# Kernel tuning notes

Hardware: AMD Instinct MI355X
Metric: run time of the kernel (lower is better)

The kernel has to match this reference:

```python
import jax, jax.numpy as jnp
import numpy as np

NEG_SLOPE = 0.2
EPS = 1e-16

N_NODES = 100000
N_EDGES = 1600000
IN_CH = 128
HEADS = 4
OUT_CH = 32


def setup_inputs() -> dict:
    key = jax.random.key(0)
    k1, k2, k3, k4, k5 = jax.random.split(key, 5)
    x = jax.random.normal(k1, (N_NODES, IN_CH), dtype=jnp.float32)
    edge_index = jax.random.randint(k2, (2, N_EDGES), 0, N_NODES, dtype=jnp.int64)
    glorot = (6.0 / (IN_CH + HEADS * OUT_CH)) ** 0.5
    W_l = jax.random.uniform(k3, (IN_CH, HEADS * OUT_CH), jnp.float32, -glorot, glorot)
    W_r = jax.random.uniform(k4, (IN_CH, HEADS * OUT_CH), jnp.float32, -glorot, glorot)
    ga = (6.0 / (OUT_CH + 1)) ** 0.5
    att = jax.random.uniform(k5, (HEADS, OUT_CH), jnp.float32, -ga, ga)
    bias = jnp.zeros((HEADS * OUT_CH,), dtype=jnp.float32)
    return {"x": x, "edge_index": edge_index, "W_l": W_l, "W_r": W_r, "att": att, "bias": bias}


def reference(x, edge_index, W_l, W_r, att, bias):
    # GATv2Conv forward (PyG semantics, concat=True, add_self_loops=False)
    N = x.shape[0]
    H, C = att.shape
    src, dst = edge_index[0], edge_index[1]

    x_l = (x @ W_l).reshape(N, H, C)  # source transform
    x_r = (x @ W_r).reshape(N, H, C)  # target transform

    # per-edge attention logits: e_ij = att . leaky_relu(x_l[j] + x_r[i])
    h = x_l[src] + x_r[dst]                      # [E, H, C]
    e = jnp.einsum('ehc,hc->eh', jax.nn.leaky_relu(h, NEG_SLOPE), att)  # [E, H]

    # segment softmax over edges grouped by destination node
    m = jax.ops.segment_max(e, dst, num_segments=N)      # [N, H]
    e_exp = jnp.exp(e - m[dst])                          # [E, H]
    denom = jax.ops.segment_sum(e_exp, dst, num_segments=N)  # [N, H]
    alpha = e_exp / (denom[dst] + EPS)                   # [E, H]

    # attention-weighted message aggregation
    msg = x_l[src] * alpha[:, :, None]                   # [E, H, C]
    out = jax.ops.segment_sum(msg, dst, num_segments=N)  # [N, H, C]
    return out.reshape(N, H * C) + bias
```

## Files before the change

### kernel.cpp

```cpp
#include <hip/hip_runtime.h>
#include <hip/hip_bf16.h>
#include <cstdint>
#include <cstddef>


#define NEG_SLOPE 0.2f
#define EPS_F 1e-16f
#define NRANGE 8
#define NCHUNK 64
#define SORT_B 1024
#define MAX_RSZ 12512

typedef __attribute__((ext_vector_type(8))) short bf16x8;
typedef __attribute__((ext_vector_type(4))) float f32x4;

static __device__ __forceinline__ unsigned f2bf(float f) {
    unsigned u = __float_as_uint(f);
    return (u + 0x7fffu + ((u >> 16) & 1u)) >> 16;
}
static __device__ __forceinline__ float bf2f(unsigned h) {
    return __uint_as_float(h << 16);
}

__global__ __launch_bounds__(SORT_B) void histW_k(const int* __restrict__ dst, int E, int N,
                                                  int rsz, int chunk_e,
                                                  unsigned* __restrict__ g,
                                                  const float* __restrict__ Wl,
                                                  const float* __restrict__ Wr,
                                                  unsigned short* __restrict__ Wtl,
                                                  unsigned short* __restrict__ Wtr) {
    if (blockIdx.x == NRANGE * NCHUNK) {
        for (int mat = 0; mat < 2; ++mat) {
            const float* W = mat ? Wr : Wl;
            unsigned short* Wt = mat ? Wtr : Wtl;
            for (int i = 0; i < 16; ++i) {
                int idx = (int)threadIdx.x + i * SORT_B;
                int k = idx >> 7, n = idx & 127;
                Wt[n * 128 + k] = (unsigned short)f2bf(W[idx]);
            }
        }
        return;
    }
    __shared__ unsigned lcnt[MAX_RSZ];
    const int r = blockIdx.x & (NRANGE - 1);
    const int c = blockIdx.x >> 3;
    const unsigned r_lo = (unsigned)(r * rsz);
    const int e0 = c * chunk_e;
    const int e1 = min(e0 + chunk_e, E);

    for (int i = threadIdx.x; i < rsz; i += SORT_B) lcnt[i] = 0u;
    __syncthreads();
    for (int e = e0 + (int)threadIdx.x; e < e1; e += SORT_B) {
        unsigned dd = (unsigned)dst[e] - r_lo;
        if (dd < (unsigned)rsz) atomicAdd(&lcnt[dd], 1u);
    }
    __syncthreads();
    unsigned* gc = g + (size_t)c * N + r_lo;
    int lim = min(rsz, N - (int)r_lo);
    for (int i = threadIdx.x; i < lim; i += SORT_B) gc[i] = lcnt[i];
}

#define LROW 136
__global__ __launch_bounds__(256) void mfma_gemm_k(const float* __restrict__ A,
                                                   const unsigned short* __restrict__ Wtl,
                                                   const unsigned short* __restrict__ Wtr,
                                                   unsigned short* __restrict__ xl,
                                                   unsigned short* __restrict__ xr,
                                                   int nrows) {
    __shared__ unsigned short As[64 * LROW];
    __shared__ unsigned short Ws[128 * LROW];
    const int tid = threadIdx.x;
    const int wave = tid >> 6, lane = tid & 63;
    const int quad = lane >> 4, m16 = lane & 15;
    const int row0 = blockIdx.x * 64;

#pragma unroll
    for (int i = 0; i < 8; ++i) {
        int idx = tid + i * 256;
        int r = idx >> 5, c4 = idx & 31;
        int gr = row0 + r;
        gr = gr < nrows ? gr : nrows - 1;
        float4 v = *(const float4*)(A + (size_t)gr * 128 + c4 * 4);
        ushort4 b;
        b.x = (unsigned short)f2bf(v.x);
        b.y = (unsigned short)f2bf(v.y);
        b.z = (unsigned short)f2bf(v.z);
        b.w = (unsigned short)f2bf(v.w);
        *(ushort4*)(&As[r * LROW + c4 * 4]) = b;
    }
#pragma unroll
    for (int i = 0; i < 8; ++i) {
        int idx = tid + i * 256;
        int n = idx >> 4, kq = idx & 15;
        *(uint4*)(&Ws[n * LROW + kq * 8]) = *(const uint4*)(Wtl + n * 128 + kq * 8);
    }
    __syncthreads();

    bf16x8 af[4];
#pragma unroll
    for (int ks = 0; ks < 4; ++ks)
        af[ks] = *(const bf16x8*)(&As[(wave * 16 + m16) * LROW + ks * 32 + quad * 8]);

    f32x4 acc[8];
#pragma unroll
    for (int ct = 0; ct < 8; ++ct) acc[ct] = (f32x4){0.f, 0.f, 0.f, 0.f};
#pragma unroll
    for (int ct = 0; ct < 8; ++ct)
#pragma unroll
        for (int ks = 0; ks < 4; ++ks) {
            bf16x8 bf = *(const bf16x8*)(&Ws[(ct * 16 + m16) * LROW + ks * 32 + quad * 8]);
            acc[ct] = __builtin_amdgcn_mfma_f32_16x16x32_bf16(af[ks], bf, acc[ct], 0, 0, 0);
        }
#pragma unroll
    for (int ct = 0; ct < 8; ++ct)
#pragma unroll
        for (int r = 0; r < 4; ++r) {
            int grow = row0 + wave * 16 + quad * 4 + r;
            if (grow < nrows) xl[(size_t)grow * 128 + ct * 16 + m16] = (unsigned short)f2bf(acc[ct][r]);
        }

    __syncthreads();
#pragma unroll
    for (int i = 0; i < 8; ++i) {
        int idx = tid + i * 256;
        int n = idx >> 4, kq = idx & 15;
        *(uint4*)(&Ws[n * LROW + kq * 8]) = *(const uint4*)(Wtr + n * 128 + kq * 8);
    }
    __syncthreads();

#pragma unroll
    for (int ct = 0; ct < 8; ++ct) acc[ct] = (f32x4){0.f, 0.f, 0.f, 0.f};
#pragma unroll
    for (int ct = 0; ct < 8; ++ct)
#pragma unroll
        for (int ks = 0; ks < 4; ++ks) {
            bf16x8 bf = *(const bf16x8*)(&Ws[(ct * 16 + m16) * LROW + ks * 32 + quad * 8]);
            acc[ct] = __builtin_amdgcn_mfma_f32_16x16x32_bf16(af[ks], bf, acc[ct], 0, 0, 0);
        }
#pragma unroll
    for (int ct = 0; ct < 8; ++ct)
#pragma unroll
        for (int r = 0; r < 4; ++r) {
            int grow = row0 + wave * 16 + quad * 4 + r;
            if (grow < nrows) xr[(size_t)grow * 128 + ct * 16 + m16] = (unsigned short)f2bf(acc[ct][r]);
        }
}

__global__ __launch_bounds__(256) void colsum_k(const unsigned* __restrict__ g, int N,
                                                int* __restrict__ cnt) {
    int d = blockIdx.x * 256 + threadIdx.x;
    if (d >= N) return;
    unsigned s = 0;
#pragma unroll
    for (int c = 0; c < NCHUNK; ++c) s += g[(size_t)c * N + d];
    cnt[d] = (int)s;
}

#define SCAN_B 256
__global__ __launch_bounds__(SCAN_B) void scanA_k(const int* __restrict__ cnt, int n,
                                                  int* __restrict__ row_start,
                                                  int* __restrict__ bsum) {
    const int tid = threadIdx.x, lane = tid & 63, wid = tid >> 6;
    const int g = blockIdx.x * SCAN_B + tid;
    int v = (g < n) ? cnt[g] : 0;
    int inc = v;
#pragma unroll
    for (int d = 1; d < 64; d <<= 1) {
        int t = __shfl_up(inc, d);
        if (lane >= d) inc += t;
    }
    __shared__ int wsum[SCAN_B / 64];
    if (lane == 63) wsum[wid] = inc;
    __syncthreads();
    int add = 0;
    for (int w = 0; w < wid; ++w) add += wsum[w];
    inc += add;
    if (g < n) row_start[g] = inc - v;
    if (tid == SCAN_B - 1) bsum[blockIdx.x] = inc;
}

__global__ __launch_bounds__(512) void scanB_k(int* __restrict__ bsum, int nb) {
    const int tid = threadIdx.x, lane = tid & 63, wid = tid >> 6;
    int v = (tid < nb) ? bsum[tid] : 0;
    int inc = v;
#pragma unroll
    for (int d = 1; d < 64; d <<= 1) {
        int t = __shfl_up(inc, d);
        if (lane >= d) inc += t;
    }
    __shared__ int wsum[8];
    if (lane == 63) wsum[wid] = inc;
    __syncthreads();
    int add = 0;
    for (int w = 0; w < wid; ++w) add += wsum[w];
    inc += add;
    if (tid < nb) bsum[tid] = inc - v;
}

__global__ __launch_bounds__(SCAN_B) void scanC_k(int* __restrict__ row_start,
                                                  const int* __restrict__ bsum,
                                                  int n, int E,
                                                  int* __restrict__ src_sorted) {
    const int g = blockIdx.x * SCAN_B + threadIdx.x;
    if (g < n) row_start[g] += bsum[blockIdx.x];
    if (g == 0) row_start[n] = E;
    if (blockIdx.x == 0 && threadIdx.x < 8) src_sorted[E + threadIdx.x] = 0;
}

__global__ __launch_bounds__(256) void cbase_k(const unsigned* __restrict__ g,
                                               const int* __restrict__ row_start, int N,
                                               unsigned* __restrict__ base) {
    int d = blockIdx.x * 256 + threadIdx.x;
    if (d >= N) return;
    unsigned run = (unsigned)row_start[d];
#pragma unroll
    for (int c = 0; c < NCHUNK; ++c) {
        base[(size_t)c * N + d] = run;
        run += g[(size_t)c * N + d];
    }
}

__global__ __launch_bounds__(SORT_B) void scat_k(const int* __restrict__ src,
                                                 const int* __restrict__ dst, int E, int N,
                                                 int rsz, int chunk_e,
                                                 const unsigned* __restrict__ base,
                                                 int* __restrict__ src_sorted) {
    __shared__ unsigned lcur[MAX_RSZ];
    const int r = blockIdx.x & (NRANGE - 1);
    const int c = blockIdx.x >> 3;
    const unsigned r_lo = (unsigned)(r * rsz);
    const int e0 = c * chunk_e;
    const int e1 = min(e0 + chunk_e, E);

    const unsigned* bc = base + (size_t)c * N + r_lo;
    int lim = min(rsz, N - (int)r_lo);
    for (int i = threadIdx.x; i < lim; i += SORT_B) lcur[i] = bc[i];
    __syncthreads();

    for (int e = e0 + (int)threadIdx.x; e < e1; e += SORT_B) {
        unsigned dd = (unsigned)dst[e] - r_lo;
        if (dd < (unsigned)rsz) {
            unsigned pos = atomicAdd(&lcur[dd], 1u);
            src_sorted[pos] = src[e];
        }
    }
}

__global__ __launch_bounds__(256) void agg_k(const unsigned* __restrict__ xlb,
                                             const unsigned* __restrict__ xrb,
                                             const float* __restrict__ att,
                                             const float* __restrict__ bias,
                                             const int* __restrict__ row_start,
                                             const int* __restrict__ src_sorted,
                                             int n, float* __restrict__ out) {
    const int wave = threadIdx.x >> 6;
    const int lane = threadIdx.x & 63;
    const int i = blockIdx.x * 4 + wave;
    if (i >= n) return;

    const int idx  = lane & 31;
    const int half = lane >> 5;

    uint2 xr2 = *(const uint2*)(xrb + (size_t)i * 64 + idx * 2);
    float xr0 = bf2f(xr2.x & 0xffffu), xr1 = bf2f(xr2.x >> 16);
    float xr2f = bf2f(xr2.y & 0xffffu), xr3 = bf2f(xr2.y >> 16);
    float4 at4 = *(const float4*)(att + idx * 4);

    const int k0 = row_start[i];
    const int k1 = row_start[i + 1];

    float l = 0.f, A0 = 0.f, A1 = 0.f, A2 = 0.f, A3 = 0.f;

    for (int k = k0; k < k1; k += 8) {
        const int kb = k + 4 * half;
        int s[4];
#pragma unroll
        for (int u = 0; u < 4; ++u) s[u] = src_sorted[kb + u];
        uint2 v[4];
#pragma unroll
        for (int u = 0; u < 4; ++u) v[u] = *(const uint2*)(xlb + (size_t)s[u] * 64 + idx * 2);
#pragma unroll
        for (int u = 0; u < 4; ++u) {
            float x0 = bf2f(v[u].x & 0xffffu), x1 = bf2f(v[u].x >> 16);
            float x2 = bf2f(v[u].y & 0xffffu), x3 = bf2f(v[u].y >> 16);
            float h0 = x0 + xr0, h1 = x1 + xr1, h2 = x2 + xr2f, h3 = x3 + xr3;
            h0 = fmaxf(h0, NEG_SLOPE * h0);
            h1 = fmaxf(h1, NEG_SLOPE * h1);
            h2 = fmaxf(h2, NEG_SLOPE * h2);
            h3 = fmaxf(h3, NEG_SLOPE * h3);
            float p = fmaf(at4.x, h0, at4.y * h1) + fmaf(at4.z, h2, at4.w * h3);
            p += __shfl_xor(p, 1);
            p += __shfl_xor(p, 2);
            p += __shfl_xor(p, 4);
            float w = (kb + u < k1) ? __expf(p) : 0.f;
            l += w;
            A0 = fmaf(w, x0, A0);
            A1 = fmaf(w, x1, A1);
            A2 = fmaf(w, x2, A2);
            A3 = fmaf(w, x3, A3);
        }
    }

    l  += __shfl_xor(l, 32);
    A0 += __shfl_xor(A0, 32);
    A1 += __shfl_xor(A1, 32);
    A2 += __shfl_xor(A2, 32);
    A3 += __shfl_xor(A3, 32);

    if (half == 0) {
        float inv = 1.f / (l + EPS_F);
        float4 b4 = *(const float4*)(bias + idx * 4);
        float4 o = {fmaf(A0, inv, b4.x), fmaf(A1, inv, b4.y),
                    fmaf(A2, inv, b4.z), fmaf(A3, inv, b4.w)};
        *(float4*)(out + (size_t)i * 128 + idx * 4) = o;
    }
}

extern "C" void kernel_launch(void* const* d_in, const int* in_sizes, int n_in,
                              void* d_out, int out_size, void* d_ws, size_t ws_size,
                              hipStream_t stream) {
    const float* x    = (const float*)d_in[0];
    const int*   ei   = (const int*)d_in[1];
    const float* W_l  = (const float*)d_in[2];
    const float* W_r  = (const float*)d_in[3];
    const float* att  = (const float*)d_in[4];
    const float* bias = (const float*)d_in[5];
    float* out = (float*)d_out;

    const int N = in_sizes[0] / 128;
    const int E = in_sizes[1] / 2;
    const int* src = ei;
    const int* dst = ei + E;

    char* ws = (char*)d_ws;
    size_t off = 0;
    auto alloc = [&](size_t bytes) {
        void* p = ws + off;
        off += (bytes + 15) & ~(size_t)15;
        return p;
    };
    unsigned* xlb     = (unsigned*)alloc((size_t)N * 64 * 4);
    unsigned* xrb     = (unsigned*)alloc((size_t)N * 64 * 4);
    unsigned* g       = (unsigned*)alloc((size_t)NCHUNK * N * 4);
    unsigned* base    = (unsigned*)alloc((size_t)NCHUNK * N * 4);
    int* cnt          = (int*)alloc((size_t)N * 4);
    int* row_start    = (int*)alloc((size_t)(N + 1) * 4);
    const int nsb = (N + SCAN_B - 1) / SCAN_B;
    int* bsum         = (int*)alloc((size_t)nsb * 4);
    int* src_sorted   = (int*)alloc((size_t)(E + 8) * 4);
    unsigned short* Wtl = (unsigned short*)alloc((size_t)128 * 128 * 2);
    unsigned short* Wtr = (unsigned short*)alloc((size_t)128 * 128 * 2);
    (void)ws_size;

    const int rsz = (N + NRANGE - 1) / NRANGE;
    const int chunk_e = (E + NCHUNK - 1) / NCHUNK;

    histW_k<<<NRANGE * NCHUNK + 1, SORT_B, 0, stream>>>(dst, E, N, rsz, chunk_e, g,
                                                        W_l, W_r, Wtl, Wtr);

    const int gB = (N + 63) / 64;
    mfma_gemm_k<<<gB, 256, 0, stream>>>(x, Wtl, Wtr,
                                        (unsigned short*)xlb, (unsigned short*)xrb, N);

    colsum_k<<<(N + 255) / 256, 256, 0, stream>>>(g, N, cnt);
    scanA_k<<<nsb, SCAN_B, 0, stream>>>(cnt, N, row_start, bsum);
    scanB_k<<<1, 512, 0, stream>>>(bsum, nsb);
    scanC_k<<<nsb, SCAN_B, 0, stream>>>(row_start, bsum, N, E, src_sorted);
    cbase_k<<<(N + 255) / 256, 256, 0, stream>>>(g, row_start, N, base);

    scat_k<<<NRANGE * NCHUNK, SORT_B, 0, stream>>>(src, dst, E, N, rsz, chunk_e,
                                                   base, src_sorted);

    agg_k<<<(N + 3) / 4, 256, 0, stream>>>(xlb, xrb, att, bias, row_start, src_sorted, N, out);
}
```

Measured before the change: 294.7 us.

## Replace chunked LDS histogram sort with global-atomic counting sort

Replaces the two-level range/chunk histogram (per-chunk LDS counts, column sums, per-chunk bases) with a direct global-atomic histogram over destinations and a global-atomic scatter. This removes the large NCHUNK×N intermediate arrays and the colsum/cbase passes, cutting memory traffic and kernel launches. The cost is heavy global atomic contention on about 1.6M edges. The order of edges within each segment also becomes nondeterministic, which can change the floating-point summation order in aggregation.

After: 412.8 us. +40.0%, slower.

```diff
diff --git a/kernel.cpp b/kernel.cpp
--- a/kernel.cpp
+++ b/kernel.cpp
@@ -6,10 +6,6 @@
 
 #define NEG_SLOPE 0.2f
 #define EPS_F 1e-16f
-#define NRANGE 8
-#define NCHUNK 64
-#define SORT_B 1024
-#define MAX_RSZ 12512
 
 typedef __attribute__((ext_vector_type(8))) short bf16x8;
 typedef __attribute__((ext_vector_type(4))) float f32x4;
@@ -22,42 +18,42 @@
     return __uint_as_float(h << 16);
 }
 
-__global__ __launch_bounds__(SORT_B) void histW_k(const int* __restrict__ dst, int E, int N,
-                                                  int rsz, int chunk_e,
-                                                  unsigned* __restrict__ g,
-                                                  const float* __restrict__ Wl,
-                                                  const float* __restrict__ Wr,
-                                                  unsigned short* __restrict__ Wtl,
-                                                  unsigned short* __restrict__ Wtr) {
-    if (blockIdx.x == NRANGE * NCHUNK) {
-        for (int mat = 0; mat < 2; ++mat) {
-            const float* W = mat ? Wr : Wl;
-            unsigned short* Wt = mat ? Wtr : Wtl;
-            for (int i = 0; i < 16; ++i) {
-                int idx = (int)threadIdx.x + i * SORT_B;
-                int k = idx >> 7, n = idx & 127;
-                Wt[n * 128 + k] = (unsigned short)f2bf(W[idx]);
-            }
-        }
+__global__ __launch_bounds__(256) void zeroW_k(int* __restrict__ cnt, int N,
+                                               const float* __restrict__ Wl,
+                                               const float* __restrict__ Wr,
+                                               unsigned short* __restrict__ Wtl,
+                                               unsigned short* __restrict__ Wtr) {
+    const int nzb = (N + 255) >> 8;
+    if ((int)blockIdx.x < nzb) {
+        int i = blockIdx.x * 256 + (int)threadIdx.x;
+        if (i < N) cnt[i] = 0;
         return;
     }
-    __shared__ unsigned lcnt[MAX_RSZ];
-    const int r = blockIdx.x & (NRANGE - 1);
-    const int c = blockIdx.x >> 3;
-    const unsigned r_lo = (unsigned)(r * rsz);
-    const int e0 = c * chunk_e;
-    const int e1 = min(e0 + chunk_e, E);
-
-    for (int i = threadIdx.x; i < rsz; i += SORT_B) lcnt[i] = 0u;
-    __syncthreads();
-    for (int e = e0 + (int)threadIdx.x; e < e1; e += SORT_B) {
-        unsigned dd = (unsigned)dst[e] - r_lo;
-        if (dd < (unsigned)rsz) atomicAdd(&lcnt[dd], 1u);
-    }
-    __syncthreads();
-    unsigned* gc = g + (size_t)c * N + r_lo;
-    int lim = min(rsz, N - (int)r_lo);
-    for (int i = threadIdx.x; i < lim; i += SORT_B) gc[i] = lcnt[i];
+    for (int mat = 0; mat < 2; ++mat) {
+        const float* W = mat ? Wr : Wl;
+        unsigned short* Wt = mat ? Wtr : Wtl;
+        for (int i = 0; i < 64; ++i) {
+            int idx = (int)threadIdx.x + i * 256;
+            int k = idx >> 7, n = idx & 127;
+            Wt[n * 128 + k] = (unsigned short)f2bf(W[idx]);
+        }
+    }
+}
+
+__global__ __launch_bounds__(256) void hist_k(const int* __restrict__ dst, int E,
+                                              int* __restrict__ cnt) {
+    const int E4 = E >> 2;
+    int i = blockIdx.x * 256 + (int)threadIdx.x;
+    if (i < E4) {
+        int4 d = ((const int4*)dst)[i];
+        atomicAdd(&cnt[d.x], 1);
+        atomicAdd(&cnt[d.y], 1);
+        atomicAdd(&cnt[d.z], 1);
+        atomicAdd(&cnt[d.w], 1);
+    }
+    if (i == 0) {
+        for (int e = E4 << 2; e < E; ++e) atomicAdd(&cnt[dst[e]], 1);
+    }
 }
 
 #define LROW 136
@@ -146,16 +142,6 @@
         }
 }
 
-__global__ __launch_bounds__(256) void colsum_k(const unsigned* __restrict__ g, int N,
-                                                int* __restrict__ cnt) {
-    int d = blockIdx.x * 256 + threadIdx.x;
-    if (d >= N) return;
-    unsigned s = 0;
-#pragma unroll
-    for (int c = 0; c < NCHUNK; ++c) s += g[(size_t)c * N + d];
-    cnt[d] = (int)s;
-}
-
 #define SCAN_B 256
 __global__ __launch_bounds__(SCAN_B) void scanA_k(const int* __restrict__ cnt, int n,
                                                   int* __restrict__ row_start,
@@ -200,48 +186,36 @@
 __global__ __launch_bounds__(SCAN_B) void scanC_k(int* __restrict__ row_start,
                                                   const int* __restrict__ bsum,
                                                   int n, int E,
-                                                  int* __restrict__ src_sorted) {
+                                                  int* __restrict__ src_sorted,
+                                                  int* __restrict__ gcur) {
     const int g = blockIdx.x * SCAN_B + threadIdx.x;
-    if (g < n) row_start[g] += bsum[blockIdx.x];
+    if (g < n) {
+        int v = row_start[g] + bsum[blockIdx.x];
+        row_start[g] = v;
+        gcur[g] = v;
+    }
     if (g == 0) row_start[n] = E;
     if (blockIdx.x == 0 && threadIdx.x < 8) src_sorted[E + threadIdx.x] = 0;
 }
 
-__global__ __launch_bounds__(256) void cbase_k(const unsigned* __restrict__ g,
-                                               const int* __restrict__ row_start, int N,
-                                               unsigned* __restrict__ base) {
-    int d = blockIdx.x * 256 + threadIdx.x;
-    if (d >= N) return;
-    unsigned run = (unsigned)row_start[d];
-#pragma unroll
-    for (int c = 0; c < NCHUNK; ++c) {
-        base[(size_t)c * N + d] = run;
-        run += g[(size_t)c * N + d];
-    }
-}
-
-__global__ __launch_bounds__(SORT_B) void scat_k(const int* __restrict__ src,
-                                                 const int* __restrict__ dst, int E, int N,
-                                                 int rsz, int chunk_e,
-                                                 const unsigned* __restrict__ base,
-                                                 int* __restrict__ src_sorted) {
-    __shared__ unsigned lcur[MAX_RSZ];
-    const int r = blockIdx.x & (NRANGE - 1);
-    const int c = blockIdx.x >> 3;
-    const unsigned r_lo = (unsigned)(r * rsz);
-    const int e0 = c * chunk_e;
-    const int e1 = min(e0 + chunk_e, E);
-
-    const unsigned* bc = base + (size_t)c * N + r_lo;
-    int lim = min(rsz, N - (int)r_lo);
-    for (int i = threadIdx.x; i < lim; i += SORT_B) lcur[i] = bc[i];
-    __syncthreads();
-
-    for (int e = e0 + (int)threadIdx.x; e < e1; e += SORT_B) {
-        unsigned dd = (unsigned)dst[e] - r_lo;
-        if (dd < (unsigned)rsz) {
-            unsigned pos = atomicAdd(&lcur[dd], 1u);
-            src_sorted[pos] = src[e];
+__global__ __launch_bounds__(256) void scat_k(const int* __restrict__ src,
+                                              const int* __restrict__ dst, int E,
+                                              int* __restrict__ gcur,
+                                              int* __restrict__ src_sorted) {
+    const int E4 = E >> 2;
+    int i = blockIdx.x * 256 + (int)threadIdx.x;
+    if (i < E4) {
+        int4 d = ((const int4*)dst)[i];
+        int4 s = ((const int4*)src)[i];
+        int p0 = atomicAdd(&gcur[d.x], 1); src_sorted[p0] = s.x;
+        int p1 = atomicAdd(&gcur[d.y], 1); src_sorted[p1] = s.y;
+        int p2 = atomicAdd(&gcur[d.z], 1); src_sorted[p2] = s.z;
+        int p3 = atomicAdd(&gcur[d.w], 1); src_sorted[p3] = s.w;
+    }
+    if (i == 0) {
+        for (int e = E4 << 2; e < E; ++e) {
+            int p = atomicAdd(&gcur[dst[e]], 1);
+            src_sorted[p] = src[e];
         }
     }
 }
@@ -341,10 +315,9 @@
     };
     unsigned* xlb     = (unsigned*)alloc((size_t)N * 64 * 4);
     unsigned* xrb     = (unsigned*)alloc((size_t)N * 64 * 4);
-    unsigned* g       = (unsigned*)alloc((size_t)NCHUNK * N * 4);
-    unsigned* base    = (unsigned*)alloc((size_t)NCHUNK * N * 4);
     int* cnt          = (int*)alloc((size_t)N * 4);
     int* row_start    = (int*)alloc((size_t)(N + 1) * 4);
+    int* gcur         = (int*)alloc((size_t)N * 4);
     const int nsb = (N + SCAN_B - 1) / SCAN_B;
     int* bsum         = (int*)alloc((size_t)nsb * 4);
     int* src_sorted   = (int*)alloc((size_t)(E + 8) * 4);
@@ -352,24 +325,21 @@
     unsigned short* Wtr = (unsigned short*)alloc((size_t)128 * 128 * 2);
     (void)ws_size;
 
-    const int rsz = (N + NRANGE - 1) / NRANGE;
-    const int chunk_e = (E + NCHUNK - 1) / NCHUNK;
-
-    histW_k<<<NRANGE * NCHUNK + 1, SORT_B, 0, stream>>>(dst, E, N, rsz, chunk_e, g,
-                                                        W_l, W_r, Wtl, Wtr);
+    const int nzb = (N + 255) / 256;
+    zeroW_k<<<nzb + 1, 256, 0, stream>>>(cnt, N, W_l, W_r, Wtl, Wtr);
+
+    const int neb = ((E >> 2) + 255) / 256;
+    hist_k<<<neb, 256, 0, stream>>>(dst, E, cnt);
 
     const int gB = (N + 63) / 64;
     mfma_gemm_k<<<gB, 256, 0, stream>>>(x, Wtl, Wtr,
                                         (unsigned short*)xlb, (unsigned short*)xrb, N);
 
-    colsum_k<<<(N + 255) / 256, 256, 0, stream>>>(g, N, cnt);
     scanA_k<<<nsb, SCAN_B, 0, stream>>>(cnt, N, row_start, bsum);
     scanB_k<<<1, 512, 0, stream>>>(bsum, nsb);
-    scanC_k<<<nsb, SCAN_B, 0, stream>>>(row_start, bsum, N, E, src_sorted);
-    cbase_k<<<(N + 255) / 256, 256, 0, stream>>>(g, row_start, N, base);
-
-    scat_k<<<NRANGE * NCHUNK, SORT_B, 0, stream>>>(src, dst, E, N, rsz, chunk_e,
-                                                   base, src_sorted);
+    scanC_k<<<nsb, SCAN_B, 0, stream>>>(row_start, bsum, N, E, src_sorted, gcur);
+
+    scat_k<<<neb, 256, 0, stream>>>(src, dst, E, gcur, src_sorted);
 
     agg_k<<<(N + 3) / 4, 256, 0, stream>>>(xlb, xrb, att, bias, row_start, src_sorted, N, out);
 }
```
